# Kernel optimization log

Measured on AMD Instinct MI355X. Metric: run time of the kernel, lower is better.

## Reference

```python
import jax, jax.numpy as jnp
import numpy as np

IN, OUT, EDGE_FEAT = 32, 32, 16
B, N = 8, 128            # batch, nodes per graph; E = B*N*N edges
H1, H2, H3 = 128, 256, 128  # NNet hidden sizes (nmp_qc default)


def _linear_params(key, n_in, n_out):
    kw, kb = jax.random.split(key)
    s = 1.0 / np.sqrt(n_in)
    W = jax.random.uniform(kw, (n_in, n_out), jnp.float32, -s, s)
    b = jax.random.uniform(kb, (n_out,), jnp.float32, -s, s)
    return W, b


def setup_inputs() -> dict:
    key = jax.random.key(0)
    ks = jax.random.split(key, 8)
    h_v = jax.random.normal(ks[0], (B, N, IN), jnp.float32)
    h_w = jax.random.normal(ks[1], (B * N, IN), jnp.float32)
    e_vw = jax.random.normal(ks[2], (B * N * N, EDGE_FEAT), jnp.float32)
    W1, b1 = _linear_params(ks[3], EDGE_FEAT, H1)
    W2, b2 = _linear_params(ks[4], H1, H2)
    W3, b3 = _linear_params(ks[5], H2, H3)
    W4, b4 = _linear_params(ks[6], H3, IN * OUT)
    return {"h_v": h_v, "h_w": h_w, "e_vw": e_vw,
            "W1": W1, "b1": b1, "W2": W2, "b2": b2,
            "W3": W3, "b3": b3, "W4": W4, "b4": b4}


def reference(h_v, h_w, e_vw, W1, b1, W2, b2, W3, b3, W4, b4):
    # Edge-conditioned weight generator (NNet MLP with ReLU hidden layers)
    x = jax.nn.relu(e_vw @ W1 + b1)
    x = jax.nn.relu(x @ W2 + b2)
    x = jax.nn.relu(x @ W3 + b3)
    edge_output = x @ W4 + b4                      # (E, out*in)
    edge_output = edge_output.reshape(-1, OUT, IN)  # (E, out, in)

    # h_w_rows: expand h_w (B*N, in) with a trailing dim of size h_v.size(1)=N,
    # then flatten to rows of length `in` (exact replica of the torch view).
    n_v = h_v.shape[1]
    h_w_rows = jnp.broadcast_to(h_w[:, :, None],
                                (h_w.shape[0], h_w.shape[1], n_v))
    h_w_rows = h_w_rows.reshape(-1, IN)            # (E, in)

    # bmm of per-edge (out, in) matrix with (in,) vector, then squeeze
    m_new = jnp.einsum('eoi,ei->eo', edge_output, h_w_rows)  # (E, out)
    return m_new
```

## Files before the change

kernel.cpp:

```cpp
#include <hip/hip_runtime.h>


typedef _Float16 f16;
typedef _Float16 f16x8 __attribute__((ext_vector_type(8)));
typedef float f32x4 __attribute__((ext_vector_type(4)));

#define OFF_W1S 0
#define OFF_W2S 4096
#define OFF_W3S 36864
#define OFF_W4S 69632
#define WS_HALFS 73728

union U16x8 { struct { uint2 lo, hi; } p; f16x8 v; };

__global__ void prep_kernel(const float* __restrict__ W1, const float* __restrict__ W2,
                            const float* __restrict__ W3, const float* __restrict__ W4,
                            const float* __restrict__ b4, f16* __restrict__ wsh,
                            float* __restrict__ b4r) {
  int t = blockIdx.x * 256 + threadIdx.x;
  if (t < 4096) {
    int j = t & 7, l = (t >> 3) & 63, ct = t >> 9;
    int k = ((l >> 4) & 3) * 8 + j, c = ct * 16 + (l & 15);
    wsh[OFF_W1S + t] = (k < 16) ? (f16)W1[k * 128 + c] : (f16)0.f;
  } else if (t < 36864) {
    int s = t - 4096;
    int j = s & 7, l = (s >> 3) & 63, kt = (s >> 9) & 3, ct = s >> 11;
    int k = kt * 32 + ((l >> 4) & 3) * 8 + j, c = ct * 16 + (l & 15);
    wsh[t] = (f16)W2[k * 256 + c];
  } else if (t < 69632) {
    int s = t - 36864;
    int j = s & 7, l = (s >> 3) & 63, kt = (s >> 9) & 7, ct = s >> 12;
    int k = kt * 32 + ((l >> 4) & 3) * 8 + j, c = ct * 16 + (l & 15);
    wsh[t] = (f16)W3[k * 128 + c];
  } else if (t < 73728) {
    int s = t - 69632;
    int j = s & 7, l = (s >> 3) & 63, kt = (s >> 9) & 3, ct = s >> 11;
    int k = kt * 32 + ((l >> 4) & 3) * 8 + j, o = ct * 16 + (l & 15);
    float a = 0.f;
#pragma unroll
    for (int i = 0; i < 32; ++i) a += W4[k * 1024 + o * 32 + i];
    wsh[t] = (f16)a;
  }
  if (t < 32) {
    float a = 0.f;
#pragma unroll
    for (int i = 0; i < 32; ++i) a += b4[t * 32 + i];
    b4r[t] = a;
  }
}

__global__ __launch_bounds__(256, 3) void mlp_mfma_kernel(
    const float* __restrict__ e_vw, const float* __restrict__ h_w,
    const float* __restrict__ b1, const float* __restrict__ b2,
    const float* __restrict__ b3,
    const f16* __restrict__ wsh, const float* __restrict__ b4r,
    float* __restrict__ out) {
  __shared__ f16 P[64 * 132];
  __shared__ f16 Q[64 * 260];

  const int l  = threadIdx.x & 63;
  const int w  = threadIdx.x >> 6;
  const int e0 = l & 15;
  const int kg = l >> 4;
  const size_t row0 = (size_t)blockIdx.x * 64;

  {
    int rl = threadIdx.x >> 2;
    int c4 = (threadIdx.x & 3) * 4;
    float4 v = *reinterpret_cast<const float4*>(e_vw + (row0 + rl) * 16 + c4);
    union { f16 h[4]; uint2 u; } pk;
    pk.h[0] = (f16)v.x; pk.h[1] = (f16)v.y; pk.h[2] = (f16)v.z; pk.h[3] = (f16)v.w;
    *reinterpret_cast<uint2*>(Q + rl * 36 + c4) = pk.u;
    uint2 z; z.x = 0u; z.y = 0u;
    *reinterpret_cast<uint2*>(Q + rl * 36 + 16 + c4) = z;
  }
  __syncthreads();

  {
    const f16x8* wp = (const f16x8*)(wsh + OFF_W1S);
    f16x8 bfr[2];
#pragma unroll
    for (int c = 0; c < 2; ++c) bfr[c] = wp[(2 * w + c) * 64 + l];
#pragma unroll
    for (int t = 0; t < 4; ++t) {
      const f16* pa = Q + (t * 16 + e0) * 36 + kg * 8;
      U16x8 a; a.p.lo = *(const uint2*)pa; a.p.hi = *(const uint2*)(pa + 4);
#pragma unroll
      for (int c = 0; c < 2; ++c) {
        f32x4 acc = {0.f, 0.f, 0.f, 0.f};
        acc = __builtin_amdgcn_mfma_f32_16x16x32_f16(a.v, bfr[c], acc, 0, 0, 0);
        int col = (2 * w + c) * 16 + e0;
        float bias = b1[col];
#pragma unroll
        for (int r = 0; r < 4; ++r)
          P[(t * 16 + kg * 4 + r) * 132 + col] = (f16)fmaxf(acc[r] + bias, 0.f);
      }
    }
  }
  __syncthreads();

  {
    const f16x8* wp = (const f16x8*)(wsh + OFF_W2S);
    f16x8 bfr[16];
#pragma unroll
    for (int c = 0; c < 4; ++c)
#pragma unroll
      for (int kt = 0; kt < 4; ++kt)
        bfr[c * 4 + kt] = wp[((4 * w + c) * 4 + kt) * 64 + l];
#pragma unroll
    for (int t = 0; t < 4; ++t) {
      const f16* pa = P + (t * 16 + e0) * 132 + kg * 8;
      U16x8 a[4];
#pragma unroll
      for (int kt = 0; kt < 4; ++kt) {
        a[kt].p.lo = *(const uint2*)(pa + kt * 32);
        a[kt].p.hi = *(const uint2*)(pa + kt * 32 + 4);
      }
#pragma unroll
      for (int c = 0; c < 4; ++c) {
        f32x4 acc = {0.f, 0.f, 0.f, 0.f};
#pragma unroll
        for (int kt = 0; kt < 4; ++kt)
          acc = __builtin_amdgcn_mfma_f32_16x16x32_f16(a[kt].v, bfr[c * 4 + kt], acc, 0, 0, 0);
        int col = (4 * w + c) * 16 + e0;
        float bias = b2[col];
#pragma unroll
        for (int r = 0; r < 4; ++r)
          Q[(t * 16 + kg * 4 + r) * 260 + col] = (f16)fmaxf(acc[r] + bias, 0.f);
      }
    }
  }
  __syncthreads();

  {
    const f16x8* wp = (const f16x8*)(wsh + OFF_W3S);
    f16x8 bfr[16];
#pragma unroll
    for (int c = 0; c < 2; ++c)
#pragma unroll
      for (int kt = 0; kt < 8; ++kt)
        bfr[c * 8 + kt] = wp[((2 * w + c) * 8 + kt) * 64 + l];
#pragma unroll
    for (int t = 0; t < 4; ++t) {
      const f16* pa = Q + (t * 16 + e0) * 260 + kg * 8;
      U16x8 a[8];
#pragma unroll
      for (int kt = 0; kt < 8; ++kt) {
        a[kt].p.lo = *(const uint2*)(pa + kt * 32);
        a[kt].p.hi = *(const uint2*)(pa + kt * 32 + 4);
      }
#pragma unroll
      for (int c = 0; c < 2; ++c) {
        f32x4 acc = {0.f, 0.f, 0.f, 0.f};
#pragma unroll
        for (int kt = 0; kt < 8; ++kt)
          acc = __builtin_amdgcn_mfma_f32_16x16x32_f16(a[kt].v, bfr[c * 8 + kt], acc, 0, 0, 0);
        int col = (2 * w + c) * 16 + e0;
        float bias = b3[col];
#pragma unroll
        for (int r = 0; r < 4; ++r)
          P[(t * 16 + kg * 4 + r) * 132 + col] = (f16)fmaxf(acc[r] + bias, 0.f);
      }
    }
  }
  __syncthreads();

  {
    const f16x8* wp = (const f16x8*)(wsh + OFF_W4S);
    const int ct = w & 1;
    const int tb = (w >> 1) * 2;
    f16x8 bfr[4];
#pragma unroll
    for (int kt = 0; kt < 4; ++kt) bfr[kt] = wp[(ct * 4 + kt) * 64 + l];
#pragma unroll
    for (int ti = 0; ti < 2; ++ti) {
      int t = tb + ti;
      const f16* pa = P + (t * 16 + e0) * 132 + kg * 8;
      U16x8 a[4];
#pragma unroll
      for (int kt = 0; kt < 4; ++kt) {
        a[kt].p.lo = *(const uint2*)(pa + kt * 32);
        a[kt].p.hi = *(const uint2*)(pa + kt * 32 + 4);
      }
      f32x4 acc = {0.f, 0.f, 0.f, 0.f};
#pragma unroll
      for (int kt = 0; kt < 4; ++kt)
        acc = __builtin_amdgcn_mfma_f32_16x16x32_f16(a[kt].v, bfr[kt], acc, 0, 0, 0);
      int col = ct * 16 + e0;
      float bb = b4r[col];
#pragma unroll
      for (int r = 0; r < 4; ++r) {
        size_t e = row0 + t * 16 + kg * 4 + r;
        float s = h_w[(e >> 7) * 32 + ((e & 127) >> 2)];
        out[e * 32 + col] = s * (acc[r] + bb);
      }
    }
  }
}

extern "C" void kernel_launch(void* const* d_in, const int* in_sizes, int n_in,
                              void* d_out, int out_size, void* d_ws, size_t ws_size,
                              hipStream_t stream) {
  const float* h_w  = (const float*)d_in[1];
  const float* e_vw = (const float*)d_in[2];
  const float* W1   = (const float*)d_in[3];
  const float* b1   = (const float*)d_in[4];
  const float* W2   = (const float*)d_in[5];
  const float* b2   = (const float*)d_in[6];
  const float* W3   = (const float*)d_in[7];
  const float* b3   = (const float*)d_in[8];
  const float* W4   = (const float*)d_in[9];
  const float* b4   = (const float*)d_in[10];
  float* out = (float*)d_out;

  f16*   wsh = (f16*)d_ws;
  float* b4r = (float*)((char*)d_ws + (size_t)WS_HALFS * 2);

  const int E = in_sizes[2] / 16;

  hipLaunchKernelGGL(prep_kernel, dim3(288), dim3(256), 0, stream,
                     W1, W2, W3, W4, b4, wsh, b4r);
  hipLaunchKernelGGL(mlp_mfma_kernel, dim3(E / 64), dim3(256), 0, stream,
                     e_vw, h_w, b1, b2, b3, wsh, b4r, out);
}
```

Before: 35.29 us.

## Transpose MFMA operands for packed row-contiguous stores, fold b1, prefetch weights

Swaps the A and B operands of every MFMA so each lane's four accumulator values are contiguous columns of one row. The ReLU results can then be packed with cvt_pkrtz into 8-byte LDS stores, and the final output is written as float4 instead of scattered scalar stores. The first-layer bias is folded into the padded K dimension through a constant-one input column. Each layer's weight fragments are now loaded before the preceding barrier so global loads overlap the sync. Risks include LDS bank conflicts on the new store pattern and round-toward-zero conversion instead of round-to-nearest.

```diff
diff --git a/kernel.cpp b/kernel.cpp
--- a/kernel.cpp
+++ b/kernel.cpp
@@ -3,6 +3,7 @@
 
 typedef _Float16 f16;
 typedef _Float16 f16x8 __attribute__((ext_vector_type(8)));
+typedef __fp16 fp16x2 __attribute__((ext_vector_type(2)));
 typedef float f32x4 __attribute__((ext_vector_type(4)));
 
 #define OFF_W1S 0
@@ -12,16 +13,18 @@
 #define WS_HALFS 73728
 
 union U16x8 { struct { uint2 lo, hi; } p; f16x8 v; };
-
-__global__ void prep_kernel(const float* __restrict__ W1, const float* __restrict__ W2,
-                            const float* __restrict__ W3, const float* __restrict__ W4,
-                            const float* __restrict__ b4, f16* __restrict__ wsh,
-                            float* __restrict__ b4r) {
+union U32x2 { fp16x2 h2[2]; uint2 u; };
+
+__global__ void prep_kernel(const float* __restrict__ W1, const float* __restrict__ b1,
+                            const float* __restrict__ W2, const float* __restrict__ W3,
+                            const float* __restrict__ W4, const float* __restrict__ b4,
+                            f16* __restrict__ wsh, float* __restrict__ b4r) {
   int t = blockIdx.x * 256 + threadIdx.x;
   if (t < 4096) {
     int j = t & 7, l = (t >> 3) & 63, ct = t >> 9;
     int k = ((l >> 4) & 3) * 8 + j, c = ct * 16 + (l & 15);
-    wsh[OFF_W1S + t] = (k < 16) ? (f16)W1[k * 128 + c] : (f16)0.f;
+    wsh[OFF_W1S + t] = (k < 16) ? (f16)W1[k * 128 + c]
+                                : (k == 16 ? (f16)b1[c] : (f16)0.f);
   } else if (t < 36864) {
     int s = t - 4096;
     int j = s & 7, l = (s >> 3) & 63, kt = (s >> 9) & 3, ct = s >> 11;
@@ -51,8 +54,7 @@
 
 __global__ __launch_bounds__(256, 3) void mlp_mfma_kernel(
     const float* __restrict__ e_vw, const float* __restrict__ h_w,
-    const float* __restrict__ b1, const float* __restrict__ b2,
-    const float* __restrict__ b3,
+    const float* __restrict__ b2, const float* __restrict__ b3,
     const f16* __restrict__ wsh, const float* __restrict__ b4r,
     float* __restrict__ out) {
   __shared__ f16 P[64 * 132];
@@ -71,16 +73,19 @@
     union { f16 h[4]; uint2 u; } pk;
     pk.h[0] = (f16)v.x; pk.h[1] = (f16)v.y; pk.h[2] = (f16)v.z; pk.h[3] = (f16)v.w;
     *reinterpret_cast<uint2*>(Q + rl * 36 + c4) = pk.u;
-    uint2 z; z.x = 0u; z.y = 0u;
-    *reinterpret_cast<uint2*>(Q + rl * 36 + 16 + c4) = z;
-  }
-  __syncthreads();
-
-  {
-    const f16x8* wp = (const f16x8*)(wsh + OFF_W1S);
-    f16x8 bfr[2];
-#pragma unroll
-    for (int c = 0; c < 2; ++c) bfr[c] = wp[(2 * w + c) * 64 + l];
+    union { f16 h[4]; uint2 u; } z;
+    z.h[0] = (c4 == 0) ? (f16)1.f : (f16)0.f; z.h[1] = (f16)0.f;
+    z.h[2] = (f16)0.f; z.h[3] = (f16)0.f;
+    *reinterpret_cast<uint2*>(Q + rl * 36 + 16 + c4) = z.u;
+  }
+
+  const f16x8* wp1 = (const f16x8*)(wsh + OFF_W1S);
+  f16x8 bfr1[2];
+#pragma unroll
+  for (int c = 0; c < 2; ++c) bfr1[c] = wp1[(2 * w + c) * 64 + l];
+  __syncthreads();
+
+  {
 #pragma unroll
     for (int t = 0; t < 4; ++t) {
       const f16* pa = Q + (t * 16 + e0) * 36 + kg * 8;
@@ -88,25 +93,28 @@
 #pragma unroll
       for (int c = 0; c < 2; ++c) {
         f32x4 acc = {0.f, 0.f, 0.f, 0.f};
-        acc = __builtin_amdgcn_mfma_f32_16x16x32_f16(a.v, bfr[c], acc, 0, 0, 0);
-        int col = (2 * w + c) * 16 + e0;
-        float bias = b1[col];
-#pragma unroll
-        for (int r = 0; r < 4; ++r)
-          P[(t * 16 + kg * 4 + r) * 132 + col] = (f16)fmaxf(acc[r] + bias, 0.f);
-      }
-    }
-  }
-  __syncthreads();
-
-  {
-    const f16x8* wp = (const f16x8*)(wsh + OFF_W2S);
-    f16x8 bfr[16];
+        acc = __builtin_amdgcn_mfma_f32_16x16x32_f16(bfr1[c], a.v, acc, 0, 0, 0);
+        U32x2 o;
+        o.h2[0] = __builtin_amdgcn_cvt_pkrtz(fmaxf(acc[0], 0.f), fmaxf(acc[1], 0.f));
+        o.h2[1] = __builtin_amdgcn_cvt_pkrtz(fmaxf(acc[2], 0.f), fmaxf(acc[3], 0.f));
+        *reinterpret_cast<uint2*>(P + (t * 16 + e0) * 132 + (2 * w + c) * 16 + kg * 4) = o.u;
+      }
+    }
+  }
+  const f16x8* wp2 = (const f16x8*)(wsh + OFF_W2S);
+  f16x8 bfr2[16];
+#pragma unroll
+  for (int c = 0; c < 4; ++c)
+#pragma unroll
+    for (int kt = 0; kt < 4; ++kt)
+      bfr2[c * 4 + kt] = wp2[((4 * w + c) * 4 + kt) * 64 + l];
+  __syncthreads();
+
+  {
+    float4 bb[4];
 #pragma unroll
     for (int c = 0; c < 4; ++c)
-#pragma unroll
-      for (int kt = 0; kt < 4; ++kt)
-        bfr[c * 4 + kt] = wp[((4 * w + c) * 4 + kt) * 64 + l];
+      bb[c] = *reinterpret_cast<const float4*>(b2 + (4 * w + c) * 16 + kg * 4);
 #pragma unroll
     for (int t = 0; t < 4; ++t) {
       const f16* pa = P + (t * 16 + e0) * 132 + kg * 8;
@@ -121,25 +129,30 @@
         f32x4 acc = {0.f, 0.f, 0.f, 0.f};
 #pragma unroll
         for (int kt = 0; kt < 4; ++kt)
-          acc = __builtin_amdgcn_mfma_f32_16x16x32_f16(a[kt].v, bfr[c * 4 + kt], acc, 0, 0, 0);
-        int col = (4 * w + c) * 16 + e0;
-        float bias = b2[col];
-#pragma unroll
-        for (int r = 0; r < 4; ++r)
-          Q[(t * 16 + kg * 4 + r) * 260 + col] = (f16)fmaxf(acc[r] + bias, 0.f);
-      }
-    }
-  }
-  __syncthreads();
-
-  {
-    const f16x8* wp = (const f16x8*)(wsh + OFF_W3S);
-    f16x8 bfr[16];
+          acc = __builtin_amdgcn_mfma_f32_16x16x32_f16(bfr2[c * 4 + kt], a[kt].v, acc, 0, 0, 0);
+        U32x2 o;
+        o.h2[0] = __builtin_amdgcn_cvt_pkrtz(fmaxf(acc[0] + bb[c].x, 0.f),
+                                             fmaxf(acc[1] + bb[c].y, 0.f));
+        o.h2[1] = __builtin_amdgcn_cvt_pkrtz(fmaxf(acc[2] + bb[c].z, 0.f),
+                                             fmaxf(acc[3] + bb[c].w, 0.f));
+        *reinterpret_cast<uint2*>(Q + (t * 16 + e0) * 260 + (4 * w + c) * 16 + kg * 4) = o.u;
+      }
+    }
+  }
+  const f16x8* wp3 = (const f16x8*)(wsh + OFF_W3S);
+  f16x8 bfr3[16];
+#pragma unroll
+  for (int c = 0; c < 2; ++c)
+#pragma unroll
+    for (int kt = 0; kt < 8; ++kt)
+      bfr3[c * 8 + kt] = wp3[((2 * w + c) * 8 + kt) * 64 + l];
+  __syncthreads();
+
+  {
+    float4 bb[2];
 #pragma unroll
     for (int c = 0; c < 2; ++c)
-#pragma unroll
-      for (int kt = 0; kt < 8; ++kt)
-        bfr[c * 8 + kt] = wp[((2 * w + c) * 8 + kt) * 64 + l];
+      bb[c] = *reinterpret_cast<const float4*>(b3 + (2 * w + c) * 16 + kg * 4);
 #pragma unroll
     for (int t = 0; t < 4; ++t) {
       const f16* pa = Q + (t * 16 + e0) * 260 + kg * 8;
@@ -154,24 +167,26 @@
         f32x4 acc = {0.f, 0.f, 0.f, 0.f};
 #pragma unroll
         for (int kt = 0; kt < 8; ++kt)
-          acc = __builtin_amdgcn_mfma_f32_16x16x32_f16(a[kt].v, bfr[c * 8 + kt], acc, 0, 0, 0);
-        int col = (2 * w + c) * 16 + e0;
-        float bias = b3[col];
-#pragma unroll
-        for (int r = 0; r < 4; ++r)
-          P[(t * 16 + kg * 4 + r) * 132 + col] = (f16)fmaxf(acc[r] + bias, 0.f);
-      }
-    }
-  }
-  __syncthreads();
-
-  {
-    const f16x8* wp = (const f16x8*)(wsh + OFF_W4S);
-    const int ct = w & 1;
-    const int tb = (w >> 1) * 2;
-    f16x8 bfr[4];
-#pragma unroll
-    for (int kt = 0; kt < 4; ++kt) bfr[kt] = wp[(ct * 4 + kt) * 64 + l];
+          acc = __builtin_amdgcn_mfma_f32_16x16x32_f16(bfr3[c * 8 + kt], a[kt].v, acc, 0, 0, 0);
+        U32x2 o;
+        o.h2[0] = __builtin_amdgcn_cvt_pkrtz(fmaxf(acc[0] + bb[c].x, 0.f),
+                                             fmaxf(acc[1] + bb[c].y, 0.f));
+        o.h2[1] = __builtin_amdgcn_cvt_pkrtz(fmaxf(acc[2] + bb[c].z, 0.f),
+                                             fmaxf(acc[3] + bb[c].w, 0.f));
+        *reinterpret_cast<uint2*>(P + (t * 16 + e0) * 132 + (2 * w + c) * 16 + kg * 4) = o.u;
+      }
+    }
+  }
+  const f16x8* wp4 = (const f16x8*)(wsh + OFF_W4S);
+  const int ct = w & 1;
+  const int tb = (w >> 1) * 2;
+  f16x8 bfr4[4];
+#pragma unroll
+  for (int kt = 0; kt < 4; ++kt) bfr4[kt] = wp4[(ct * 4 + kt) * 64 + l];
+  __syncthreads();
+
+  {
+    float4 bb = *reinterpret_cast<const float4*>(b4r + ct * 16 + kg * 4);
 #pragma unroll
     for (int ti = 0; ti < 2; ++ti) {
       int t = tb + ti;
@@ -185,15 +200,13 @@
       f32x4 acc = {0.f, 0.f, 0.f, 0.f};
 #pragma unroll
       for (int kt = 0; kt < 4; ++kt)
-        acc = __builtin_amdgcn_mfma_f32_16x16x32_f16(a[kt].v, bfr[kt], acc, 0, 0, 0);
-      int col = ct * 16 + e0;
-      float bb = b4r[col];
-#pragma unroll
-      for (int r = 0; r < 4; ++r) {
-        size_t e = row0 + t * 16 + kg * 4 + r;
-        float s = h_w[(e >> 7) * 32 + ((e & 127) >> 2)];
-        out[e * 32 + col] = s * (acc[r] + bb);
-      }
+        acc = __builtin_amdgcn_mfma_f32_16x16x32_f16(bfr4[kt], a[kt].v, acc, 0, 0, 0);
+      size_t e = row0 + t * 16 + e0;
+      float s = h_w[(e >> 7) * 32 + ((e & 127) >> 2)];
+      float4 st;
+      st.x = s * (acc[0] + bb.x); st.y = s * (acc[1] + bb.y);
+      st.z = s * (acc[2] + bb.z); st.w = s * (acc[3] + bb.w);
+      *reinterpret_cast<float4*>(out + e * 32 + ct * 16 + kg * 4) = st;
     }
   }
 }
@@ -219,7 +232,7 @@
   const int E = in_sizes[2] / 16;
 
   hipLaunchKernelGGL(prep_kernel, dim3(288), dim3(256), 0, stream,
-                     W1, W2, W3, W4, b4, wsh, b4r);
+                     W1, b1, W2, W3, W4, b4, wsh, b4r);
   hipLaunchKernelGGL(mlp_mfma_kernel, dim3(E / 64), dim3(256), 0, stream,
-                     e_vw, h_w, b1, b2, b3, wsh, b4r, out);
+                     e_vw, h_w, b2, b3, wsh, b4r, out);
 }
```

New measurement: 32.63 us. 7.5% less time.
